# Performance work log

Hardware: AMD Instinct MI355X
Metric: run time of the kernel (lower is better)

The kernel has to match this reference:

```python
import jax, jax.numpy as jnp
import numpy as np

B, N, DIN, DOUT = 8, 2048, 256, 256
ALPHA = 0.2  # leaky relu slope
EPS = 1e-6


def setup_inputs() -> dict:
    key = jax.random.key(0)
    k1, k2, k3, k4 = jax.random.split(key, 4)
    h = jax.random.normal(k1, (B, N, DIN), dtype=jnp.float32)
    adj = jax.random.uniform(k2, (B, N, N), dtype=jnp.float32)
    # xavier_uniform with gain=1.414
    gain = 1.414
    limW = gain * np.sqrt(6.0 / (DIN + DOUT))
    W = jax.random.uniform(k3, (DIN, DOUT), minval=-limW, maxval=limW, dtype=jnp.float32)
    lima = gain * np.sqrt(6.0 / (2 * DOUT + 1))
    a = jax.random.uniform(k4, (2 * DOUT, 1), minval=-lima, maxval=lima, dtype=jnp.float32)
    return {"h": h, "adj": adj, "W": W, "a": a}


def reference(h, adj, W, a):
    # Wh: [B, N, DOUT]
    Wh = jnp.einsum("bnd,df->bnf", h, W)
    # Split additive attention: cat([Wh_i, Wh_j]) @ a == Wh_i @ a1 + Wh_j @ a2
    a1 = a[:DOUT, 0]   # [DOUT]
    a2 = a[DOUT:, 0]   # [DOUT]
    s1 = Wh @ a1       # [B, N] score contribution of source node i
    s2 = Wh @ a2       # [B, N] score contribution of target node j
    e = s1[:, :, None] + s2[:, None, :]           # [B, N, N]
    e = jnp.where(e > 0, e, ALPHA * e)            # leaky relu
    e = e + jnp.log(adj + EPS)                    # soft adjacency mask
    alpha_w = jax.nn.softmax(e, axis=-1)          # [B, N, N]
    # dropout is identity in eval / deterministic reference
    h_prime = jnp.einsum("bij,bjf->bif", alpha_w, Wh)
    return h_prime
```

## Files before the change

kernel.cpp:

```cpp
#include <hip/hip_runtime.h>
#include <hip/hip_bf16.h>
#include <stdint.h>

#define ALPHA_ 0.2f
#define EPS_   1e-6f

typedef __attribute__((ext_vector_type(8))) short  short8;
typedef __attribute__((ext_vector_type(4))) float  float4v;

static __device__ __forceinline__ unsigned short f2bf(float x) {
    union { float f; unsigned int u; } c; c.f = x;
    return (unsigned short)((c.u + 0x7fffu + ((c.u >> 16) & 1u)) >> 16);
}

__global__ __launch_bounds__(256) void k_wt(const float* __restrict__ W,
                                            unsigned short* __restrict__ WTs) {
    const int g  = blockIdx.x * 256 + threadIdx.x;
    const int fb = g >> 9, kc = (g >> 6) & 7, l = g & 63;
    const int m = l & 15, quad = l >> 4;
    const int f = fb * 16 + m, d0 = kc * 32 + quad * 8;
    unsigned short v[8];
#pragma unroll
    for (int i = 0; i < 8; ++i) v[i] = f2bf(W[(d0 + i) * 256 + f]);
    uint4 o;
    o.x = (unsigned)v[0] | ((unsigned)v[1] << 16);
    o.y = (unsigned)v[2] | ((unsigned)v[3] << 16);
    o.z = (unsigned)v[4] | ((unsigned)v[5] << 16);
    o.w = (unsigned)v[6] | ((unsigned)v[7] << 16);
    *(uint4*)(WTs + (size_t)g * 8) = o;
}

__global__ __launch_bounds__(512) void k_wh(const float* __restrict__ h,
                                            const unsigned short* __restrict__ WTs,
                                            const float* __restrict__ a,
                                            unsigned short* __restrict__ WhS,
                                            float* __restrict__ s1g,
                                            float* __restrict__ s2g) {
    __shared__ __align__(16) unsigned short A_lds[32][264];
    __shared__ __align__(16) unsigned short T_lds[256][40];
    __shared__ float s1p[32], s2p[32];
    const int t    = threadIdx.x;
    const int lane = t & 63;
    const int wv   = t >> 6;
    const int m    = lane & 15;
    const int quad = lane >> 4;
    const int r0   = blockIdx.x * 32;
    const int b    = blockIdx.x >> 6;
    const int jc   = blockIdx.x & 63;
    const int j0   = r0 & 2047;

    if (t < 32) { s1p[t] = 0.f; s2p[t] = 0.f; }

#pragma unroll
    for (int k = 0; k < 4; ++k) {
        const int flat = t + k * 512;
        const int r  = flat >> 6;
        const int d4 = flat & 63;
        float4v hv = *(const float4v*)(h + (size_t)(r0 + r) * 256 + d4 * 4);
        uint2 pk;
        pk.x = (unsigned)f2bf(hv.x) | ((unsigned)f2bf(hv.y) << 16);
        pk.y = (unsigned)f2bf(hv.z) | ((unsigned)f2bf(hv.w) << 16);
        *(uint2*)&A_lds[r][d4 * 4] = pk;
    }
    __syncthreads();

    const int fbase = wv * 32;
    float4v acc[2][2];
#pragma unroll
    for (int it = 0; it < 2; ++it)
#pragma unroll
        for (int ft = 0; ft < 2; ++ft)
#pragma unroll
            for (int r = 0; r < 4; ++r) acc[it][ft][r] = 0.f;

    const unsigned short* wtb = WTs + (size_t)(wv * 2) * 4096 + lane * 8;

#pragma unroll
    for (int kc = 0; kc < 8; ++kc) {
        short8 af0 = *(const short8*)&A_lds[m][kc * 32 + quad * 8];
        short8 af1 = *(const short8*)&A_lds[16 + m][kc * 32 + quad * 8];
#pragma unroll
        for (int ft = 0; ft < 2; ++ft) {
            short8 bf = *(const short8*)(wtb + (size_t)ft * 4096 + kc * 512);
            acc[0][ft] = __builtin_amdgcn_mfma_f32_16x16x32_bf16(af0, bf, acc[0][ft], 0, 0, 0);
            acc[1][ft] = __builtin_amdgcn_mfma_f32_16x16x32_bf16(af1, bf, acc[1][ft], 0, 0, 0);
        }
    }

    float a1v[2], a2v[2];
#pragma unroll
    for (int ft = 0; ft < 2; ++ft) {
        a1v[ft] = a[fbase + ft * 16 + m];
        a2v[ft] = a[256 + fbase + ft * 16 + m];
    }
#pragma unroll
    for (int it = 0; it < 2; ++it) {
#pragma unroll
        for (int reg = 0; reg < 4; ++reg) {
            float v1 = 0.f, v2 = 0.f;
#pragma unroll
            for (int ft = 0; ft < 2; ++ft) {
                const float c = acc[it][ft][reg];
                v1 = fmaf(c, a1v[ft], v1);
                v2 = fmaf(c, a2v[ft], v2);
            }
            v1 += __shfl_xor(v1, 1); v2 += __shfl_xor(v2, 1);
            v1 += __shfl_xor(v1, 2); v2 += __shfl_xor(v2, 2);
            v1 += __shfl_xor(v1, 4); v2 += __shfl_xor(v2, 4);
            v1 += __shfl_xor(v1, 8); v2 += __shfl_xor(v2, 8);
            if (m == 0) {
                const int row = it * 16 + quad * 4 + reg;
                atomicAdd(&s1p[row], v1);
                atomicAdd(&s2p[row], v2);
            }
        }
    }

#pragma unroll
    for (int it = 0; it < 2; ++it)
#pragma unroll
        for (int ft = 0; ft < 2; ++ft)
#pragma unroll
            for (int reg = 0; reg < 4; ++reg)
                T_lds[fbase + ft * 16 + m][it * 16 + quad * 4 + reg] =
                    f2bf(acc[it][ft][reg]);

    __syncthreads();

#pragma unroll
    for (int e = 0; e < 2; ++e) {
        const int idx = e * 512 + t;
        const int fb = idx >> 6, l = idx & 63;
        uint4 v = *(const uint4*)&T_lds[fb * 16 + (l & 15)][(l >> 4) * 8];
        *(uint4*)(WhS + ((size_t)(b * 64 + jc) * 16 + fb) * 512 + l * 8) = v;
    }

    if (t < 32) {
        s1g[(size_t)b * 2048 + j0 + t] = s1p[t];
        s2g[(size_t)b * 2048 + j0 + t] = s2p[t];
    }
}

static __device__ __forceinline__ unsigned pk2bf(float lo, float hi) {
    float2 v; v.x = lo; v.y = hi;
    union { __hip_bfloat162 h2; unsigned u; } cv;
    cv.h2 = __float22bfloat162_rn(v);
    return cv.u;
}

static __device__ __forceinline__ uint2 pquad(float4v av, float4v s2v,
                                              float s1, float& rs) {
    float e0 = s1 + s2v.x, e1 = s1 + s2v.y, e2 = s1 + s2v.z, e3 = s1 + s2v.w;
    e0 = fmaxf(e0, ALPHA_ * e0); e1 = fmaxf(e1, ALPHA_ * e1);
    e2 = fmaxf(e2, ALPHA_ * e2); e3 = fmaxf(e3, ALPHA_ * e3);
    const float p0 = (av.x + EPS_) * __expf(e0);
    const float p1 = (av.y + EPS_) * __expf(e1);
    const float p2 = (av.z + EPS_) * __expf(e2);
    const float p3 = (av.w + EPS_) * __expf(e3);
    rs += (p0 + p1) + (p2 + p3);
    uint2 r;
    r.x = pk2bf(p0, p1);
    r.y = pk2bf(p2, p3);
    return r;
}

__global__ __launch_bounds__(512, 4) void k_attn(const float* __restrict__ adj,
                                                 const unsigned short* __restrict__ WhS,
                                                 const float* __restrict__ s1g,
                                                 const float* __restrict__ s2g,
                                                 float* __restrict__ out) {
    __shared__ __align__(16) unsigned short pbuf[2][32][268];
    __shared__ __align__(16) float s2_lds[2048];
    __shared__ float rsum_lds[32];

    const int t    = threadIdx.x;
    const int lane = t & 63;
    const int wv   = t >> 6;
    const int m    = lane & 15;
    const int quad = lane >> 4;
    const int blk  = blockIdx.x;
    const int b    = blk & 7;
    const int i0   = (blk >> 3) * 32;

    const int ip = t >> 4;
    const int jq = t & 15;

    const float* adjp = adj + (size_t)(b * 2048 + i0 + ip) * 2048 + jq * 4;
    const float  s1v  = s1g[(size_t)b * 2048 + i0 + ip];

    const int fbb = wv * 2;
    const unsigned short* whs = WhS + (size_t)b * 64 * 16 * 512;

    *(float4v*)&s2_lds[t * 4] = *(const float4v*)(s2g + (size_t)b * 2048 + t * 4);

    float4v acc[2][2];
#pragma unroll
    for (int it = 0; it < 2; ++it)
#pragma unroll
        for (int ft = 0; ft < 2; ++ft)
#pragma unroll
            for (int r = 0; r < 4; ++r) acc[it][ft][r] = 0.f;

    float rs = 0.f;

    float4v adjv[4];
#pragma unroll
    for (int c = 0; c < 4; ++c)
        adjv[c] = *(const float4v*)(adjp + c * 64);

    __syncthreads();

    for (int step = 0; step < 8; ++step) {
        const int cur = step & 1;

#pragma unroll
        for (int c = 0; c < 4; ++c) {
            float4v s2v = *(const float4v*)&s2_lds[step * 256 + c * 64 + jq * 4];
            uint2 pk = pquad(adjv[c], s2v, s1v, rs);
            *(uint2*)&pbuf[cur][ip][c * 64 + jq * 4] = pk;
        }

        __syncthreads();

        if (step < 7) {
#pragma unroll
            for (int c = 0; c < 4; ++c)
                adjv[c] = *(const float4v*)(adjp + (size_t)(step + 1) * 256 + c * 64);
        }

#pragma unroll
        for (int kc = 0; kc < 8; ++kc) {
            const unsigned short* bp =
                whs + ((size_t)((step * 8 + kc) * 16 + fbb)) * 512 + lane * 8;
            short8 bf0 = *(const short8*)bp;
            short8 bf1 = *(const short8*)(bp + 512);
            short8 af0 = *(const short8*)&pbuf[cur][m][kc * 32 + quad * 8];
            short8 af1 = *(const short8*)&pbuf[cur][16 + m][kc * 32 + quad * 8];
            acc[0][0] = __builtin_amdgcn_mfma_f32_16x16x32_bf16(af0, bf0, acc[0][0], 0, 0, 0);
            acc[0][1] = __builtin_amdgcn_mfma_f32_16x16x32_bf16(af0, bf1, acc[0][1], 0, 0, 0);
            acc[1][0] = __builtin_amdgcn_mfma_f32_16x16x32_bf16(af1, bf0, acc[1][0], 0, 0, 0);
            acc[1][1] = __builtin_amdgcn_mfma_f32_16x16x32_bf16(af1, bf1, acc[1][1], 0, 0, 0);
        }
    }

    rs += __shfl_xor(rs, 1);
    rs += __shfl_xor(rs, 2);
    rs += __shfl_xor(rs, 4);
    rs += __shfl_xor(rs, 8);
    if (jq == 0) rsum_lds[ip] = rs;
    __syncthreads();

#pragma unroll
    for (int reg = 0; reg < 4; ++reg) {
        const int row  = quad * 4 + reg;
        const float i0v = 1.0f / rsum_lds[row];
        const float i1v = 1.0f / rsum_lds[16 + row];
#pragma unroll
        for (int ft = 0; ft < 2; ++ft) {
            const int f = wv * 32 + ft * 16 + m;
            out[(size_t)(b * 2048 + i0 + row) * 256 + f]      = acc[0][ft][reg] * i0v;
            out[(size_t)(b * 2048 + i0 + 16 + row) * 256 + f] = acc[1][ft][reg] * i1v;
        }
    }
}

extern "C" void kernel_launch(void* const* d_in, const int* in_sizes, int n_in,
                              void* d_out, int out_size, void* d_ws, size_t ws_size,
                              hipStream_t stream) {
    const float* h   = (const float*)d_in[0];
    const float* adj = (const float*)d_in[1];
    const float* W   = (const float*)d_in[2];
    const float* a   = (const float*)d_in[3];
    float* out = (float*)d_out;

    unsigned short* WhS = (unsigned short*)d_ws;
    unsigned short* WTs = (unsigned short*)((char*)d_ws + 8388608);
    float*          s1  = (float*)((char*)d_ws + 8388608 + 131072);
    float*          s2  = s1 + 16384;

    k_wt  <<<dim3(32),   dim3(256), 0, stream>>>(W, WTs);
    k_wh  <<<dim3(512),  dim3(512), 0, stream>>>(h, WTs, a, WhS, s1, s2);
    k_attn<<<dim3(512),  dim3(512), 0, stream>>>(adj, WhS, s1, s2, out);
}
```

Baseline: 243.2 us.

## Halve attention step width and double-buffer adj loads across 16 steps

Reworks the attention main loop from 8 steps of 256 columns to 16 steps of 128 columns. Each thread now reads 8 contiguous adj floats, and the adj registers alternate between two sets so the next step's loads are issued before the current P computation. sched_barrier calls keep that order fixed. This shrinks the LDS P buffer, which may raise occupancy, and aims to hide global load latency. The cost is twice as many __syncthreads, and the final unconditional load wraps around to reread step 0 redundantly.

```diff
diff --git a/kernel.cpp b/kernel.cpp
--- a/kernel.cpp
+++ b/kernel.cpp
@@ -169,7 +169,7 @@
                                                  const float* __restrict__ s1g,
                                                  const float* __restrict__ s2g,
                                                  float* __restrict__ out) {
-    __shared__ __align__(16) unsigned short pbuf[2][32][268];
+    __shared__ __align__(16) unsigned short pbuf[2][32][140];
     __shared__ __align__(16) float s2_lds[2048];
     __shared__ float rsum_lds[32];
 
@@ -185,7 +185,7 @@
     const int ip = t >> 4;
     const int jq = t & 15;
 
-    const float* adjp = adj + (size_t)(b * 2048 + i0 + ip) * 2048 + jq * 4;
+    const float* adjp = adj + (size_t)(b * 2048 + i0 + ip) * 2048 + jq * 8;
     const float  s1v  = s1g[(size_t)b * 2048 + i0 + ip];
 
     const int fbb = wv * 2;
@@ -203,45 +203,63 @@
 
     float rs = 0.f;
 
-    float4v adjv[4];
-#pragma unroll
-    for (int c = 0; c < 4; ++c)
-        adjv[c] = *(const float4v*)(adjp + c * 64);
+    float4v adjA[2], adjB[2];
+    adjA[0] = *(const float4v*)(adjp);
+    adjA[1] = *(const float4v*)(adjp + 4);
 
     __syncthreads();
 
-    for (int step = 0; step < 8; ++step) {
-        const int cur = step & 1;
-
-#pragma unroll
-        for (int c = 0; c < 4; ++c) {
-            float4v s2v = *(const float4v*)&s2_lds[step * 256 + c * 64 + jq * 4];
-            uint2 pk = pquad(adjv[c], s2v, s1v, rs);
-            *(uint2*)&pbuf[cur][ip][c * 64 + jq * 4] = pk;
-        }
-
+#define PHASE_P(sp, src, buf)                                                   \
+    {                                                                           \
+        _Pragma("unroll")                                                       \
+        for (int c = 0; c < 2; ++c) {                                           \
+            float4v s2v = *(const float4v*)&s2_lds[(sp) * 128 + jq * 8 + c * 4];\
+            uint2 pk = pquad(src[c], s2v, s1v, rs);                             \
+            *(uint2*)&pbuf[buf][ip][jq * 8 + c * 4] = pk;                       \
+        }                                                                       \
+    }
+
+#define PHASE_MFMA(sp, buf)                                                     \
+    {                                                                           \
+        _Pragma("unroll")                                                       \
+        for (int kc = 0; kc < 4; ++kc) {                                        \
+            const unsigned short* bp =                                          \
+                whs + ((size_t)(((sp) * 4 + kc) * 16 + fbb)) * 512 + lane * 8;  \
+            short8 bf0 = *(const short8*)bp;                                    \
+            short8 bf1 = *(const short8*)(bp + 512);                            \
+            short8 af0 = *(const short8*)&pbuf[buf][m][kc * 32 + quad * 8];     \
+            short8 af1 = *(const short8*)&pbuf[buf][16 + m][kc * 32 + quad * 8];\
+            acc[0][0] = __builtin_amdgcn_mfma_f32_16x16x32_bf16(af0, bf0, acc[0][0], 0, 0, 0); \
+            acc[0][1] = __builtin_amdgcn_mfma_f32_16x16x32_bf16(af0, bf1, acc[0][1], 0, 0, 0); \
+            acc[1][0] = __builtin_amdgcn_mfma_f32_16x16x32_bf16(af1, bf0, acc[1][0], 0, 0, 0); \
+            acc[1][1] = __builtin_amdgcn_mfma_f32_16x16x32_bf16(af1, bf1, acc[1][1], 0, 0, 0); \
+        }                                                                       \
+    }
+
+    for (int s = 0; s < 16; s += 2) {
+        {
+            const int ns = s + 1;
+            adjB[0] = *(const float4v*)(adjp + (size_t)ns * 128);
+            adjB[1] = *(const float4v*)(adjp + (size_t)ns * 128 + 4);
+        }
+        __builtin_amdgcn_sched_barrier(0);
+        PHASE_P(s, adjA, 0)
         __syncthreads();
-
-        if (step < 7) {
-#pragma unroll
-            for (int c = 0; c < 4; ++c)
-                adjv[c] = *(const float4v*)(adjp + (size_t)(step + 1) * 256 + c * 64);
-        }
-
-#pragma unroll
-        for (int kc = 0; kc < 8; ++kc) {
-            const unsigned short* bp =
-                whs + ((size_t)((step * 8 + kc) * 16 + fbb)) * 512 + lane * 8;
-            short8 bf0 = *(const short8*)bp;
-            short8 bf1 = *(const short8*)(bp + 512);
-            short8 af0 = *(const short8*)&pbuf[cur][m][kc * 32 + quad * 8];
-            short8 af1 = *(const short8*)&pbuf[cur][16 + m][kc * 32 + quad * 8];
-            acc[0][0] = __builtin_amdgcn_mfma_f32_16x16x32_bf16(af0, bf0, acc[0][0], 0, 0, 0);
-            acc[0][1] = __builtin_amdgcn_mfma_f32_16x16x32_bf16(af0, bf1, acc[0][1], 0, 0, 0);
-            acc[1][0] = __builtin_amdgcn_mfma_f32_16x16x32_bf16(af1, bf0, acc[1][0], 0, 0, 0);
-            acc[1][1] = __builtin_amdgcn_mfma_f32_16x16x32_bf16(af1, bf1, acc[1][1], 0, 0, 0);
-        }
-    }
+        PHASE_MFMA(s, 0)
+
+        {
+            const int ns = (s + 2) & 15;
+            adjA[0] = *(const float4v*)(adjp + (size_t)ns * 128);
+            adjA[1] = *(const float4v*)(adjp + (size_t)ns * 128 + 4);
+        }
+        __builtin_amdgcn_sched_barrier(0);
+        PHASE_P(s + 1, adjB, 1)
+        __syncthreads();
+        PHASE_MFMA(s + 1, 1)
+    }
+
+#undef PHASE_P
+#undef PHASE_MFMA
 
     rs += __shfl_xor(rs, 1);
     rs += __shfl_xor(rs, 2);
```

Result: faster. 231.8 us (-4.7%).
